# Optimization experiments

Measured on AMD Instinct MI355X. Metric: run time of the kernel, lower is better.

## Reference

```python
import jax, jax.numpy as jnp
import numpy as np

H = 16  # num_attention_heads
LN_EPS = 1e-12


def setup_inputs() -> dict:
    key = jax.random.key(0)
    ks = jax.random.split(key, 13)
    S, B, D = 2048, 2, 1024
    std = 0.02
    return {
        "query_tensor": jax.random.normal(ks[0], (S, B, D), jnp.float32),
        "key_tensor": jax.random.normal(ks[1], (S, B, D), jnp.float32),
        "value_tensor": jax.random.normal(ks[2], (S, B, D), jnp.float32),
        "Wq": jax.random.normal(ks[3], (D, D), jnp.float32) * std,
        "bq": jnp.zeros((D,), jnp.float32),
        "Wk": jax.random.normal(ks[4], (D, D), jnp.float32) * std,
        "bk": jnp.zeros((D,), jnp.float32),
        "Wv": jax.random.normal(ks[5], (D, D), jnp.float32) * std,
        "bv": jnp.zeros((D,), jnp.float32),
        "Wo": jax.random.normal(ks[6], (D, D), jnp.float32) * std,
        "bo": jnp.zeros((D,), jnp.float32),
        "ln_w": jnp.ones((D,), jnp.float32),
        "ln_b": jnp.zeros((D,), jnp.float32),
    }


def _layernorm(x, w, b):
    u = jnp.mean(x, axis=-1, keepdims=True)
    s = jnp.mean(jnp.square(x - u), axis=-1, keepdims=True)
    return w * ((x - u) / jnp.sqrt(s + LN_EPS)) + b


def reference(query_tensor, key_tensor, value_tensor, Wq, bq, Wk, bk, Wv, bv, Wo, bo, ln_w, ln_b):
    S, B, D = query_tensor.shape
    dh = D // H
    # QKV projections (nn.Linear: x @ W.T + b)
    q = query_tensor @ Wq.T + bq          # (S, B, D)
    k = key_tensor @ Wk.T + bk            # (Sk, B, D)
    v = value_tensor @ Wv.T + bv          # (Sk, B, D)
    # (S, B, D) -> (B*H, S, dh)
    q = q.reshape(S, B * H, dh).transpose(1, 0, 2)
    k = k.reshape(-1, B * H, dh).transpose(1, 0, 2)
    v = v.reshape(-1, B * H, dh).transpose(1, 0, 2)
    # NOTE: original code has NO 1/sqrt(dh) scaling
    scores = jnp.einsum('nqd,nkd->nqk', q, k)            # (B*H, S, Sk)
    probs = jax.nn.softmax(scores, axis=-1)
    # dropout is identity in eval mode
    ctx = jnp.einsum('nqk,nkd->nqd', probs, v)           # (B*H, S, dh)
    ctx = ctx.transpose(1, 0, 2).reshape(S, B, D)
    # BertSelfOutput: dense + residual + LayerNorm (dropout identity)
    out = ctx @ Wo.T + bo
    return _layernorm(out + query_tensor, ln_w, ln_b)
```

## Files before the change

### kernel.cpp

```cpp
#include <hip/hip_runtime.h>

#define SEQ    2048
#define BATCH  2
#define DMODEL 1024
#define NHEAD  16
#define DH     64
#define MROWS  (SEQ*BATCH)
#define RS     (BATCH*DMODEL)
#define LN_EPS 1e-12f
#define LOG2E  1.4426950408889634f

typedef __attribute__((ext_vector_type(8))) short short8;
typedef __attribute__((ext_vector_type(4))) float floatx4;

#define AS_GLOBAL __attribute__((address_space(1)))
#define AS_LDS    __attribute__((address_space(3)))

__device__ __forceinline__ float bf2f(unsigned short s) {
    union { unsigned u; float f; } a; a.u = ((unsigned)s) << 16; return a.f;
}
__device__ __forceinline__ unsigned short f2bf(float x) {
    union { float f; unsigned u; } a; a.f = x;
    unsigned r = a.u + 0x7fffu + ((a.u >> 16) & 1u);
    return (unsigned short)(r >> 16);
}
__device__ __forceinline__ unsigned cvt_pk_bf16(float a, float b) {
    unsigned r;
    asm("v_cvt_pk_bf16_f32 %0, %1, %2" : "=v"(r) : "v"(a), "v"(b));
    return r;
}
__device__ __forceinline__ float max3f(float a, float b, float c) {
    float r;
    asm("v_max3_f32 %0, %1, %2, %3" : "=v"(r) : "v"(a), "v"(b), "v"(c));
    return r;
}
__device__ __forceinline__ float fast_exp2(float x) {
#if __has_builtin(__builtin_amdgcn_exp2f)
    return __builtin_amdgcn_exp2f(x);
#else
    return exp2f(x);
#endif
}
__device__ __forceinline__ uint4 cvt8(const float* __restrict__ p) {
    float4 x0 = *(const float4*)(p);
    float4 x1 = *(const float4*)(p + 4);
    union { uint4 u; unsigned short s[8]; } r;
    r.s[0] = f2bf(x0.x); r.s[1] = f2bf(x0.y);
    r.s[2] = f2bf(x0.z); r.s[3] = f2bf(x0.w);
    r.s[4] = f2bf(x1.x); r.s[5] = f2bf(x1.y);
    r.s[6] = f2bf(x1.z); r.s[7] = f2bf(x1.w);
    return r.u;
}
__device__ __forceinline__ uint4 cvt8s(const float* __restrict__ p, float sc) {
    float4 x0 = *(const float4*)(p);
    float4 x1 = *(const float4*)(p + 4);
    union { uint4 u; unsigned short s[8]; } r;
    r.s[0] = f2bf(x0.x*sc); r.s[1] = f2bf(x0.y*sc);
    r.s[2] = f2bf(x0.z*sc); r.s[3] = f2bf(x0.w*sc);
    r.s[4] = f2bf(x1.x*sc); r.s[5] = f2bf(x1.y*sc);
    r.s[6] = f2bf(x1.z*sc); r.s[7] = f2bf(x1.w*sc);
    return r.u;
}

__global__ void beacon_kernel(float* out, float val) {
    if (threadIdx.x == 0) out[0] = val;
}

__global__ __launch_bounds__(256)
void cvt_kernel(const float* __restrict__ s0, const float* __restrict__ s1,
                const float* __restrict__ s2, const float* __restrict__ s3,
                const float* __restrict__ s4, const float* __restrict__ s5,
                const float* __restrict__ s6,
                unsigned short* __restrict__ d0, unsigned short* __restrict__ d1,
                unsigned short* __restrict__ d2, unsigned short* __restrict__ d3,
                unsigned short* __restrict__ d4, unsigned short* __restrict__ d5,
                unsigned short* __restrict__ d6)
{
    const float* srcs[7] = {s0, s1, s2, s3, s4, s5, s6};
    unsigned short* dsts[7] = {d0, d1, d2, d3, d4, d5, d6};
    const int cnts[7] = {4194304, 4194304, 4194304, 1048576, 1048576, 1048576, 1048576};
    const float scl[7] = {1.f, 1.f, 1.f, LOG2E, 1.f, 1.f, 1.f};
    const int z = blockIdx.z;
    const float* src = srcs[z];
    unsigned short* dst = dsts[z];
    const int count = cnts[z];
    const float sc = scl[z];
    const int stride = gridDim.x * 256 * 8;
    for (int i = (blockIdx.x * 256 + threadIdx.x) * 8; i < count; i += stride)
        *(uint4*)&dst[i] = cvt8s(&src[i], sc);
}

__global__ __launch_bounds__(256)
void vt_kernel(const unsigned short* __restrict__ Vb,
               unsigned short* __restrict__ VT)
{
    __shared__ __align__(16) short T[64*72];
    const int tid = threadIdx.x;
    const int s0 = blockIdx.x * 64;
    const int bh = blockIdx.y;
    const int b = bh >> 4, h = bh & 15;

    #pragma unroll
    for (int rep = 0; rep < 2; ++rep) {
        int c = tid + rep * 256;
        int s = c >> 3, cc = c & 7;
        *(uint4*)&T[s*72 + cc*8] =
            *(const uint4*)&Vb[((s0 + s) * BATCH + b) * DMODEL + h*64 + cc*8];
    }
    __syncthreads();
    #pragma unroll
    for (int rep = 0; rep < 2; ++rep) {
        int o = tid + rep * 256;
        int d = o >> 3, sc = o & 7;
        union { uint4 u; unsigned short e[8]; } pk;
        #pragma unroll
        for (int j = 0; j < 8; ++j)
            pk.e[j] = (unsigned short)T[(sc*8 + j)*72 + d];
        *(uint4*)&VT[bh*(DH*SEQ) + d*SEQ + s0 + sc*8] = pk.u;
    }
}

template<int OUTF32>
__device__ __forceinline__ void gemm_bf16_body(
    const unsigned short* __restrict__ A,
    const unsigned short* __restrict__ W,
    const float* __restrict__ bias, float bscale,
    void* __restrict__ Cout, int m0, int n0)
{
    __shared__ __align__(16) short Alds[2][128*32];
    __shared__ __align__(16) short Blds[2][128*32];

    const int tid  = threadIdx.x;
    const int lane = tid & 63;
    const int wave = tid >> 6;
    const int lrow = lane & 15;
    const int lq   = lane >> 4;
    const int mw = (wave >> 1) * 64;
    const int nw = (wave & 1) * 64;
    const int K  = DMODEL;

    const int chunk0 = tid;
    const int chunk1 = tid + 256;
    const int row0 = chunk0 >> 2, col0 = (chunk0 & 3) << 3;
    const int row1 = chunk1 >> 2, col1 = (chunk1 & 3) << 3;
    const unsigned short* gA0 = &A[(m0 + row0) * K + col0];
    const unsigned short* gA1 = &A[(m0 + row1) * K + col1];
    const unsigned short* gB0 = &W[(n0 + row0) * K + col0];
    const unsigned short* gB1 = &W[(n0 + row1) * K + col1];

    auto stage = [&](int k0, int b) {
        __builtin_amdgcn_global_load_lds((const AS_GLOBAL unsigned int*)(gA0 + k0),
            (AS_LDS unsigned int*)&Alds[b][(wave*64)*8], 16, 0, 0);
        __builtin_amdgcn_global_load_lds((const AS_GLOBAL unsigned int*)(gA1 + k0),
            (AS_LDS unsigned int*)&Alds[b][(256 + wave*64)*8], 16, 0, 0);
        __builtin_amdgcn_global_load_lds((const AS_GLOBAL unsigned int*)(gB0 + k0),
            (AS_LDS unsigned int*)&Blds[b][(wave*64)*8], 16, 0, 0);
        __builtin_amdgcn_global_load_lds((const AS_GLOBAL unsigned int*)(gB1 + k0),
            (AS_LDS unsigned int*)&Blds[b][(256 + wave*64)*8], 16, 0, 0);
    };

    floatx4 zero = {0.f, 0.f, 0.f, 0.f};
    floatx4 acc[4][4];
    #pragma unroll
    for (int i = 0; i < 4; ++i)
        #pragma unroll
        for (int j = 0; j < 4; ++j) acc[i][j] = zero;

    stage(0, 0);
    __syncthreads();

    for (int k0 = 0; k0 < K; k0 += 32) {
        const int cur = (k0 >> 5) & 1;
        if (k0 + 32 < K) stage(k0 + 32, cur ^ 1);
        short8 af[4], bfg[4];
        #pragma unroll
        for (int mi = 0; mi < 4; ++mi)
            af[mi] = *(const short8*)&Alds[cur][(mw + mi*16 + lrow)*32 + lq*8];
        #pragma unroll
        for (int ni = 0; ni < 4; ++ni)
            bfg[ni] = *(const short8*)&Blds[cur][(nw + ni*16 + lrow)*32 + lq*8];
        #pragma unroll
        for (int mi = 0; mi < 4; ++mi)
            #pragma unroll
            for (int ni = 0; ni < 4; ++ni)
                acc[mi][ni] = __builtin_amdgcn_mfma_f32_16x16x32_bf16(af[mi], bfg[ni], acc[mi][ni], 0, 0, 0);
        __syncthreads();
    }

    #pragma unroll
    for (int mi = 0; mi < 4; ++mi) {
        #pragma unroll
        for (int ni = 0; ni < 4; ++ni) {
            int n = n0 + nw + ni*16 + lrow;
            float bv_ = bias[n] * bscale;
            #pragma unroll
            for (int r = 0; r < 4; ++r) {
                int m = m0 + mw + mi*16 + lq*4 + r;
                float v = acc[mi][ni][r] + bv_;
                if (OUTF32) ((float*)Cout)[m * DMODEL + n] = v;
                else ((unsigned short*)Cout)[m * DMODEL + n] = f2bf(v);
            }
        }
    }
}

__global__ __launch_bounds__(256)
void qkv_bf16(const unsigned short* __restrict__ qb, const unsigned short* __restrict__ kb,
              const unsigned short* __restrict__ vb,
              const unsigned short* __restrict__ Wqb, const float* __restrict__ bq,
              const unsigned short* __restrict__ Wkb, const float* __restrict__ bk,
              const unsigned short* __restrict__ Wvb, const float* __restrict__ bv,
              unsigned short* __restrict__ Qo, unsigned short* __restrict__ Ko,
              unsigned short* __restrict__ Vo)
{
    const int flat = blockIdx.x;
    const int ns = (flat & 7) * 96 + (flat >> 3);
    const int z  = ns >> 8;
    const int r  = ns & 255;
    const int n0 = (r & 7) * 128;
    const int m0 = (r >> 3) * 128;

    const unsigned short *A, *W; const float* B; unsigned short* C; float bs;
    if (z == 0)      { A = qb; W = Wqb; B = bq; C = Qo; bs = LOG2E; }
    else if (z == 1) { A = kb; W = Wkb; B = bk; C = Ko; bs = 1.f; }
    else             { A = vb; W = Wvb; B = bv; C = Vo; bs = 1.f; }
    gemm_bf16_body<0>(A, W, B, bs, C, m0, n0);
}

__global__ __launch_bounds__(256)
void oproj_bf16(const unsigned short* __restrict__ Cx,
                const unsigned short* __restrict__ Wob, const float* __restrict__ bo,
                float* __restrict__ O32)
{
    const int flat = blockIdx.x;
    const int ns = (flat & 7) * 32 + (flat >> 3);
    const int n0 = (ns & 7) * 128;
    const int m0 = (ns >> 3) * 128;
    gemm_bf16_body<1>(Cx, Wob, bo, 1.f, O32, m0, n0);
}

__global__ __launch_bounds__(256)
void qkv_mfma(const float* __restrict__ q_in, const float* __restrict__ k_in,
              const float* __restrict__ v_in,
              const float* __restrict__ Wq, const float* __restrict__ bq,
              const float* __restrict__ Wk, const float* __restrict__ bk,
              const float* __restrict__ Wv, const float* __restrict__ bv,
              unsigned short* __restrict__ Qo, unsigned short* __restrict__ Ko,
              unsigned short* __restrict__ Vo)
{
    const float *A, *W, *B; unsigned short* C;
    if (blockIdx.z == 0)      { A = q_in; W = Wq; B = bq; C = Qo; }
    else if (blockIdx.z == 1) { A = k_in; W = Wk; B = bk; C = Ko; }
    else                      { A = v_in; W = Wv; B = bv; C = Vo; }

    __shared__ __align__(16) short Alds[128*32];
    __shared__ __align__(16) short Blds[128*32];
    const int tid  = threadIdx.x;
    const int lane = tid & 63;
    const int wave = tid >> 6;
    const int lrow = lane & 15;
    const int lq   = lane >> 4;
    const int m0 = blockIdx.x * 128;
    const int n0 = blockIdx.y * 128;
    const int mw = (wave >> 1) * 64;
    const int nw = (wave & 1) * 64;
    const int K  = DMODEL;

    floatx4 zero = {0.f, 0.f, 0.f, 0.f};
    floatx4 acc[4][4];
    #pragma unroll
    for (int i = 0; i < 4; ++i)
        #pragma unroll
        for (int j = 0; j < 4; ++j) acc[i][j] = zero;

    for (int k0 = 0; k0 < K; k0 += 32) {
        #pragma unroll
        for (int rep = 0; rep < 2; ++rep) {
            int chunk = tid + rep * 256;
            int row = chunk >> 2;
            int col = (chunk & 3) << 3;
            *(uint4*)&Alds[row*32 + col] = cvt8(&A[(m0 + row) * K + k0 + col]);
            *(uint4*)&Blds[row*32 + col] = cvt8(&W[(n0 + row) * K + k0 + col]);
        }
        __syncthreads();
        short8 af[4], bfg[4];
        #pragma unroll
        for (int mi = 0; mi < 4; ++mi)
            af[mi] = *(const short8*)&Alds[(mw + mi*16 + lrow)*32 + lq*8];
        #pragma unroll
        for (int ni = 0; ni < 4; ++ni)
            bfg[ni] = *(const short8*)&Blds[(nw + ni*16 + lrow)*32 + lq*8];
        #pragma unroll
        for (int mi = 0; mi < 4; ++mi)
            #pragma unroll
            for (int ni = 0; ni < 4; ++ni)
                acc[mi][ni] = __builtin_amdgcn_mfma_f32_16x16x32_bf16(af[mi], bfg[ni], acc[mi][ni], 0, 0, 0);
        __syncthreads();
    }

    #pragma unroll
    for (int mi = 0; mi < 4; ++mi) {
        #pragma unroll
        for (int ni = 0; ni < 4; ++ni) {
            int n = n0 + nw + ni*16 + lrow;
            float bv_ = B[n];
            #pragma unroll
            for (int r = 0; r < 4; ++r) {
                int m = m0 + mw + mi*16 + lq*4 + r;
                C[m * DMODEL + n] = f2bf(acc[mi][ni][r] + bv_);
            }
        }
    }
}

__global__ __launch_bounds__(256)
void oproj_mfma(const unsigned short* __restrict__ Cx,
                const float* __restrict__ Wo, const float* __restrict__ bo,
                float* __restrict__ O32)
{
    __shared__ __align__(16) short Alds[128*32];
    __shared__ __align__(16) short Blds[128*32];
    const int tid  = threadIdx.x;
    const int lane = tid & 63;
    const int wave = tid >> 6;
    const int lrow = lane & 15;
    const int lq   = lane >> 4;
    const int m0 = blockIdx.x * 128;
    const int n0 = blockIdx.y * 128;
    const int mw = (wave >> 1) * 64;
    const int nw = (wave & 1) * 64;
    const int K  = DMODEL;

    floatx4 zero = {0.f, 0.f, 0.f, 0.f};
    floatx4 acc[4][4];
    #pragma unroll
    for (int i = 0; i < 4; ++i)
        #pragma unroll
        for (int j = 0; j < 4; ++j) acc[i][j] = zero;

    for (int k0 = 0; k0 < K; k0 += 32) {
        #pragma unroll
        for (int rep = 0; rep < 2; ++rep) {
            int chunk = tid + rep * 256;
            int row = chunk >> 2;
            int col = (chunk & 3) << 3;
            *(uint4*)&Alds[row*32 + col] = *(const uint4*)&Cx[(m0 + row) * K + k0 + col];
            *(uint4*)&Blds[row*32 + col] = cvt8(&Wo[(n0 + row) * K + k0 + col]);
        }
        __syncthreads();
        short8 af[4], bfg[4];
        #pragma unroll
        for (int mi = 0; mi < 4; ++mi)
            af[mi] = *(const short8*)&Alds[(mw + mi*16 + lrow)*32 + lq*8];
        #pragma unroll
        for (int ni = 0; ni < 4; ++ni)
            bfg[ni] = *(const short8*)&Blds[(nw + ni*16 + lrow)*32 + lq*8];
        #pragma unroll
        for (int mi = 0; mi < 4; ++mi)
            #pragma unroll
            for (int ni = 0; ni < 4; ++ni)
                acc[mi][ni] = __builtin_amdgcn_mfma_f32_16x16x32_bf16(af[mi], bfg[ni], acc[mi][ni], 0, 0, 0);
        __syncthreads();
    }

    #pragma unroll
    for (int mi = 0; mi < 4; ++mi) {
        #pragma unroll
        for (int ni = 0; ni < 4; ++ni) {
            int n = n0 + nw + ni*16 + lrow;
            float bv_ = bo[n];
            #pragma unroll
            for (int r = 0; r < 4; ++r) {
                int m = m0 + mw + mi*16 + lq*4 + r;
                O32[m * DMODEL + n] = acc[mi][ni][r] + bv_;
            }
        }
    }
}

__global__ __launch_bounds__(256)
void attn_mfma6(const unsigned short* __restrict__ Q,
                const unsigned short* __restrict__ Kg,
                const unsigned short* __restrict__ VT,
                unsigned short* __restrict__ Ctx)
{
    __shared__ __align__(16) short SMEM[20480];

    const int tid  = threadIdx.x;
    const int lane = tid & 63;
    const int wave = tid >> 6;
    const int lrow = lane & 15;
    const int lq   = lane >> 4;

    const int flat = blockIdx.x + (blockIdx.y << 5);
    const int ns   = (flat & 7) * 128 + (flat >> 3);
    const int q0 = (ns & 31) * 64;
    const int bh = ns >> 5;

    const int off = (bh >> 4) * DMODEL + (bh & 15) * DH;
    const unsigned short* VTb = VT + bh * (DH * SEQ);
    short* const psw = &SMEM[16384 + wave * 1024];

    auto stageKV = [&](int kt, int b) {
        const int kbase = kt * 64;
        short* ksb = &SMEM[b * 8192];
        short* vtb = &SMEM[b * 8192 + 4096];
        #pragma unroll
        for (int rep = 0; rep < 2; ++rep) {
            int c = rep*256 + tid;
            int r = c >> 3, cc = c & 7;
            int sw = ((cc ^ (r & 7)) << 3);
            __builtin_amdgcn_global_load_lds(
                (const AS_GLOBAL unsigned int*)&Kg[(kbase + r) * RS + off + sw],
                (AS_LDS unsigned int*)&ksb[(rep*256 + wave*64) * 8], 16, 0, 0);
            __builtin_amdgcn_global_load_lds(
                (const AS_GLOBAL unsigned int*)&VTb[r * SEQ + kbase + sw],
                (AS_LDS unsigned int*)&vtb[(rep*256 + wave*64) * 8], 16, 0, 0);
        }
    };

    stageKV(0, 0);

    const int qrow = q0 + wave*16 + lrow;
    short8 qf[2];
    qf[0] = *(const short8*)&Q[qrow * RS + off + lq*8];
    qf[1] = *(const short8*)&Q[qrow * RS + off + 32 + lq*8];

    floatx4 zero = {0.f, 0.f, 0.f, 0.f};
    float m_i = -1e30f, l_i = 0.f;
    floatx4 oacc[4];
    #pragma unroll
    for (int ni = 0; ni < 4; ++ni) oacc[ni] = zero;

    __syncthreads();

    for (int kt = 0; kt < SEQ/64; ++kt) {
        const int cur = kt & 1;
        if (kt + 1 < SEQ/64) stageKV(kt + 1, cur ^ 1);
        const short* ksb = &SMEM[cur * 8192];
        const short* vtb = &SMEM[cur * 8192 + 4096];

        floatx4 sacc[4];
        #pragma unroll
        for (int ni = 0; ni < 4; ++ni) sacc[ni] = zero;
        __builtin_amdgcn_s_setprio(1);
        #pragma unroll
        for (int ni = 0; ni < 4; ++ni) {
            #pragma unroll
            for (int kk = 0; kk < 2; ++kk) {
                int key = ni*16 + lrow;
                int cc  = kk*4 + lq;
                short8 kf = *(const short8*)&ksb[key*64 + ((cc ^ (key & 7)) << 3)];
                sacc[ni] = __builtin_amdgcn_mfma_f32_16x16x32_bf16(kf, qf[kk], sacc[ni], 0, 0, 0);
            }
        }
        __builtin_amdgcn_s_setprio(0);

        float a0 = max3f(sacc[0][0], sacc[0][1], sacc[0][2]);
        float a1 = max3f(sacc[0][3], sacc[1][0], sacc[1][1]);
        float a2 = max3f(sacc[1][2], sacc[1][3], sacc[2][0]);
        float a3 = max3f(sacc[2][1], sacc[2][2], sacc[2][3]);
        float a4 = max3f(sacc[3][0], sacc[3][1], sacc[3][2]);
        float b0 = max3f(a0, a1, a2);
        float b1 = max3f(a3, a4, sacc[3][3]);
        float mx = fmaxf(b0, b1);
        mx = fmaxf(mx, __shfl_xor(mx, 16));
        mx = fmaxf(mx, __shfl_xor(mx, 32));

        if (!__all(mx <= m_i + 8.f)) {
            float mnew = fmaxf(m_i, mx);
            float alpha = fast_exp2(m_i - mnew);
            l_i *= alpha;
            #pragma unroll
            for (int ni = 0; ni < 4; ++ni)
                #pragma unroll
                for (int r = 0; r < 4; ++r) oacc[ni][r] *= alpha;
            m_i = mnew;
        }
        float p[4][4];
        #pragma unroll
        for (int ni = 0; ni < 4; ++ni)
            #pragma unroll
            for (int r = 0; r < 4; ++r)
                p[ni][r] = fast_exp2(sacc[ni][r] - m_i);

        float s00 = (p[0][0] + p[0][1]) + (p[0][2] + p[0][3]);
        float s01 = (p[1][0] + p[1][1]) + (p[1][2] + p[1][3]);
        float s10 = (p[2][0] + p[2][1]) + (p[2][2] + p[2][3]);
        float s11 = (p[3][0] + p[3][1]) + (p[3][2] + p[3][3]);
        float psum = (s00 + s01) + (s10 + s11);
        psum += __shfl_xor(psum, 16);
        psum += __shfl_xor(psum, 32);
        l_i += psum;

        #pragma unroll
        for (int ni = 0; ni < 4; ++ni) {
            uint2 pk;
            pk.x = cvt_pk_bf16(p[ni][0], p[ni][1]);
            pk.y = cvt_pk_bf16(p[ni][2], p[ni][3]);
            int t  = ni*2 + (lq >> 1);
            int tp = t ^ (lrow & 7);
            *(uint2*)&psw[lrow*64 + tp*8 + (lq & 1)*4] = pk;
        }
        __builtin_amdgcn_wave_barrier();

        short8 pf[2];
        #pragma unroll
        for (int kk = 0; kk < 2; ++kk) {
            int t  = kk*4 + lq;
            int tp = t ^ (lrow & 7);
            pf[kk] = *(const short8*)&psw[lrow*64 + tp*8];
        }

        __builtin_amdgcn_s_setprio(1);
        #pragma unroll
        for (int ni = 0; ni < 4; ++ni) {
            #pragma unroll
            for (int kk = 0; kk < 2; ++kk) {
                int d  = ni*16 + lrow;
                int cc = kk*4 + lq;
                short8 vf = *(const short8*)&vtb[d*64 + ((cc ^ (d & 7)) << 3)];
                oacc[ni] = __builtin_amdgcn_mfma_f32_16x16x32_bf16(vf, pf[kk], oacc[ni], 0, 0, 0);
            }
        }
        __builtin_amdgcn_s_setprio(0);

        __syncthreads();
    }

    const float inv = 1.f / l_i;
    #pragma unroll
    for (int ni = 0; ni < 4; ++ni) {
        uint2 ok;
        ok.x = cvt_pk_bf16(oacc[ni][0] * inv, oacc[ni][1] * inv);
        ok.y = cvt_pk_bf16(oacc[ni][2] * inv, oacc[ni][3] * inv);
        *(uint2*)&Ctx[qrow * RS + off + ni*16 + lq*4] = ok;
    }
}

__global__ __launch_bounds__(256)
void attn_mfma2(const unsigned short* __restrict__ Q,
                const unsigned short* __restrict__ Kg,
                const unsigned short* __restrict__ V,
                unsigned short* __restrict__ Ctx)
{
    __shared__ __align__(16) short Qs[64*72];
    __shared__ __align__(16) short Ks[64*72];
    __shared__ __align__(16) short Vt[64*72];
    __shared__ __align__(16) short Ps[4][16*72];

    const int tid  = threadIdx.x;
    const int lane = tid & 63;
    const int wave = tid >> 6;
    const int lrow = lane & 15;
    const int lq   = lane >> 4;

    const int q0 = blockIdx.x * 64;
    const int bh = blockIdx.y;
    const int off = (bh >> 4) * DMODEL + (bh & 15) * DH;

    #pragma unroll
    for (int rep = 0; rep < 2; ++rep) {
        int chunk = tid + rep * 256;
        int r = chunk >> 3;
        int c = (chunk & 7) << 3;
        *(uint4*)&Qs[r*72 + c] = *(const uint4*)&Q[(q0 + r) * RS + off + c];
    }
    __syncthreads();

    short8 qf[2];
    #pragma unroll
    for (int ks = 0; ks < 2; ++ks)
        qf[ks] = *(const short8*)&Qs[(wave*16 + lrow)*72 + ks*32 + lq*8];

    floatx4 zero = {0.f, 0.f, 0.f, 0.f};
    float m_i = -1e30f, l_i = 0.f;
    floatx4 oacc[4];
    #pragma unroll
    for (int ni = 0; ni < 4; ++ni) oacc[ni] = zero;

    for (int kt = 0; kt < SEQ/64; ++kt) {
        __syncthreads();
        const int kbase = kt * 64;
        #pragma unroll
        for (int rep = 0; rep < 2; ++rep) {
            int chunk = tid + rep * 256;
            int r = chunk >> 3;
            int c = (chunk & 7) << 3;
            *(uint4*)&Ks[r*72 + c] = *(const uint4*)&Kg[(kbase + r) * RS + off + c];
            uint4 vv = *(const uint4*)&V[(kbase + r) * RS + off + c];
            union { uint4 u; short s[8]; } uv; uv.u = vv;
            int swz = (chunk & 7) << 3;
            #pragma unroll
            for (int j = 0; j < 8; ++j)
                Vt[(c + j)*72 + (r ^ swz)] = uv.s[j];
        }
        __syncthreads();

        floatx4 sacc[4];
        #pragma unroll
        for (int ni = 0; ni < 4; ++ni) sacc[ni] = zero;
        #pragma unroll
        for (int ni = 0; ni < 4; ++ni) {
            #pragma unroll
            for (int ks = 0; ks < 2; ++ks) {
                short8 kf = *(const short8*)&Ks[(ni*16 + lrow)*72 + ks*32 + lq*8];
                sacc[ni] = __builtin_amdgcn_mfma_f32_16x16x32_bf16(kf, qf[ks], sacc[ni], 0, 0, 0);
            }
        }

        float mx = sacc[0][0];
        #pragma unroll
        for (int ni = 0; ni < 4; ++ni)
            #pragma unroll
            for (int r = 0; r < 4; ++r) mx = fmaxf(mx, sacc[ni][r]);
        mx = fmaxf(mx, __shfl_xor(mx, 16));
        mx = fmaxf(mx, __shfl_xor(mx, 32));
        float mnew = fmaxf(m_i, mx);
        float alpha = __expf(m_i - mnew);
        float p[4][4];
        float psum = 0.f;
        #pragma unroll
        for (int ni = 0; ni < 4; ++ni)
            #pragma unroll
            for (int r = 0; r < 4; ++r) {
                p[ni][r] = __expf(sacc[ni][r] - mnew);
                psum += p[ni][r];
            }
        psum += __shfl_xor(psum, 16);
        psum += __shfl_xor(psum, 32);
        l_i = l_i * alpha + psum;
        m_i = mnew;
        #pragma unroll
        for (int ni = 0; ni < 4; ++ni)
            #pragma unroll
            for (int r = 0; r < 4; ++r) oacc[ni][r] *= alpha;

        #pragma unroll
        for (int ni = 0; ni < 4; ++ni) {
            uint2 pk;
            pk.x = (unsigned)f2bf(p[ni][0]) | ((unsigned)f2bf(p[ni][1]) << 16);
            pk.y = (unsigned)f2bf(p[ni][2]) | ((unsigned)f2bf(p[ni][3]) << 16);
            *(uint2*)&Ps[wave][lrow*72 + ni*16 + lq*4] = pk;
        }
        __builtin_amdgcn_wave_barrier();

        short8 pf[2];
        #pragma unroll
        for (int ks = 0; ks < 2; ++ks)
            pf[ks] = *(const short8*)&Ps[wave][lrow*72 + ks*32 + lq*8];
        #pragma unroll
        for (int ni = 0; ni < 4; ++ni) {
            #pragma unroll
            for (int ks = 0; ks < 2; ++ks) {
                int d  = ni*16 + lrow;
                int kk = ks*32 + lq*8;
                int swz = ((d >> 3) & 7) << 3;
                short8 vf = *(const short8*)&Vt[d*72 + (kk ^ swz)];
                oacc[ni] = __builtin_amdgcn_mfma_f32_16x16x32_bf16(vf, pf[ks], oacc[ni], 0, 0, 0);
            }
        }
    }

    const float inv = 1.f / l_i;
    const int q = q0 + wave*16 + lrow;
    #pragma unroll
    for (int ni = 0; ni < 4; ++ni) {
        uint2 ok;
        ok.x = (unsigned)f2bf(oacc[ni][0] * inv) | ((unsigned)f2bf(oacc[ni][1] * inv) << 16);
        ok.y = (unsigned)f2bf(oacc[ni][2] * inv) | ((unsigned)f2bf(oacc[ni][3] * inv) << 16);
        *(uint2*)&Ctx[q * RS + off + ni*16 + lq*4] = ok;
    }
}

__global__ __launch_bounds__(256)
void ln2_kernel(const float* __restrict__ O,
                const float* __restrict__ resid,
                const float* __restrict__ w,
                const float* __restrict__ bb,
                float* __restrict__ out)
{
    __shared__ float r1s[4];
    __shared__ float r2s[4];
    const int row = blockIdx.x;
    const int tid = threadIdx.x;
    const int c4 = tid * 4;

    float4 o4 = *(const float4*)&O[row * DMODEL + c4];
    float4 q4 = *(const float4*)&resid[row * DMODEL + c4];
    float x0 = o4.x + q4.x;
    float x1 = o4.y + q4.y;
    float x2 = o4.z + q4.z;
    float x3 = o4.w + q4.w;

    float s1 = x0 + x1 + x2 + x3;
    float s2 = x0*x0 + x1*x1 + x2*x2 + x3*x3;
    #pragma unroll
    for (int o = 32; o > 0; o >>= 1) {
        s1 += __shfl_xor(s1, o);
        s2 += __shfl_xor(s2, o);
    }
    if ((tid & 63) == 0) { r1s[tid >> 6] = s1; r2s[tid >> 6] = s2; }
    __syncthreads();
    float t1 = r1s[0] + r1s[1] + r1s[2] + r1s[3];
    float t2 = r2s[0] + r2s[1] + r2s[2] + r2s[3];

    const float mean = t1 * (1.f / DMODEL);
    float var = t2 * (1.f / DMODEL) - mean * mean;
    var = fmaxf(var, 0.f);
    const float rstd = rsqrtf(var + LN_EPS);

    float4 w4 = *(const float4*)&w[c4];
    float4 b4 = *(const float4*)&bb[c4];
    float4 y;
    y.x = w4.x * ((x0 - mean) * rstd) + b4.x;
    y.y = w4.y * ((x1 - mean) * rstd) + b4.y;
    y.z = w4.z * ((x2 - mean) * rstd) + b4.z;
    y.w = w4.w * ((x3 - mean) * rstd) + b4.w;
    *(float4*)&out[row * DMODEL + c4] = y;
}

extern "C" void kernel_launch(void* const* d_in, const int* in_sizes, int n_in,
                              void* d_out, int out_size, void* d_ws, size_t ws_size,
                              hipStream_t stream) {
    const float* q_in = (const float*)d_in[0];
    const float* k_in = (const float*)d_in[1];
    const float* v_in = (const float*)d_in[2];
    const float* Wq = (const float*)d_in[3];  const float* bq = (const float*)d_in[4];
    const float* Wk = (const float*)d_in[5];  const float* bk = (const float*)d_in[6];
    const float* Wv = (const float*)d_in[7];  const float* bv = (const float*)d_in[8];
    const float* Wo = (const float*)d_in[9];  const float* bo = (const float*)d_in[10];
    const float* lnw = (const float*)d_in[11]; const float* lnb = (const float*)d_in[12];

    char* wsb = (char*)d_ws;
    unsigned short* QCtx = (unsigned short*)d_out;
    float*          outF = (float*)d_out;
    dim3 blk(256);

    if (ws_size >= (48u << 20)) {
        unsigned short* qb  = (unsigned short*)(wsb);
        unsigned short* kb  = (unsigned short*)(wsb + (8u  << 20));
        unsigned short* vb  = (unsigned short*)(wsb + (16u << 20));
        unsigned short* Wqb = (unsigned short*)(wsb + (24u << 20));
        unsigned short* Wkb = (unsigned short*)(wsb + (26u << 20));
        unsigned short* Wvb = (unsigned short*)(wsb + (28u << 20));
        unsigned short* Wob = (unsigned short*)(wsb + (30u << 20));
        unsigned short* Kb  = (unsigned short*)(wsb + (32u << 20));
        unsigned short* Vb  = (unsigned short*)(wsb + (40u << 20));
        unsigned short* VT  = (unsigned short*)(wsb);
        float*          O32 = (float*)(wsb);

        cvt_kernel<<<dim3(512, 1, 7), blk, 0, stream>>>(
            q_in, k_in, v_in, Wq, Wk, Wv, Wo,
            qb, kb, vb, Wqb, Wkb, Wvb, Wob);
        qkv_bf16<<<dim3(768), blk, 0, stream>>>(
            qb, kb, vb, Wqb, bq, Wkb, bk, Wvb, bv, QCtx, Kb, Vb);
        vt_kernel<<<dim3(SEQ/64, BATCH*NHEAD), blk, 0, stream>>>(Vb, VT);
        attn_mfma6<<<dim3(SEQ/64, BATCH*NHEAD), blk, 0, stream>>>(QCtx, Kb, VT, QCtx);
        oproj_bf16<<<dim3(256), blk, 0, stream>>>(QCtx, Wob, bo, O32);
        ln2_kernel<<<dim3(MROWS), blk, 0, stream>>>(O32, q_in, lnw, lnb, outF);
    } else if (ws_size >= (16u << 20)) {
        unsigned short* Kb  = (unsigned short*)(wsb);
        unsigned short* Vb  = (unsigned short*)(wsb + (8u << 20));
        float*          O32 = (float*)(wsb);
        qkv_mfma<<<dim3(MROWS/128, DMODEL/128, 3), blk, 0, stream>>>(
            q_in, k_in, v_in, Wq, bq, Wk, bk, Wv, bv, QCtx, Kb, Vb);
        attn_mfma2<<<dim3(SEQ/64, BATCH*NHEAD), blk, 0, stream>>>(QCtx, Kb, Vb, QCtx);
        oproj_mfma<<<dim3(MROWS/128, DMODEL/128), blk, 0, stream>>>(QCtx, Wo, bo, O32);
        ln2_kernel<<<dim3(MROWS), blk, 0, stream>>>(O32, q_in, lnw, lnb, outF);
    } else {
        beacon_kernel<<<1, 64, 0, stream>>>((float*)d_out, 300.0f);
    }
}
```

Measured before the change: 250.2 us.

## Double attention query tile per block to reuse staged K/V tiles

```diff
diff --git a/kernel.cpp b/kernel.cpp
--- a/kernel.cpp
+++ b/kernel.cpp
@@ -379,12 +379,13 @@
 }
 
 __global__ __launch_bounds__(256)
-void attn_mfma6(const unsigned short* __restrict__ Q,
+void attn_mfma7(const unsigned short* __restrict__ Q,
                 const unsigned short* __restrict__ Kg,
                 const unsigned short* __restrict__ VT,
                 unsigned short* __restrict__ Ctx)
 {
-    __shared__ __align__(16) short SMEM[20480];
+    __shared__ __align__(16) short SMEM[16384];
+    __shared__ __align__(16) short PS[8192];
 
     const int tid  = threadIdx.x;
     const int lane = tid & 63;
@@ -392,14 +393,13 @@
     const int lrow = lane & 15;
     const int lq   = lane >> 4;
 
-    const int flat = blockIdx.x + (blockIdx.y << 5);
-    const int ns   = (flat & 7) * 128 + (flat >> 3);
-    const int q0 = (ns & 31) * 64;
-    const int bh = ns >> 5;
+    const int flat = blockIdx.x;
+    const int ns   = (flat & 7) * 64 + (flat >> 3);
+    const int q0 = (ns & 15) * 128;
+    const int bh = ns >> 4;
 
     const int off = (bh >> 4) * DMODEL + (bh & 15) * DH;
     const unsigned short* VTb = VT + bh * (DH * SEQ);
-    short* const psw = &SMEM[16384 + wave * 1024];
 
     auto stageKV = [&](int kt, int b) {
         const int kbase = kt * 64;
@@ -421,16 +421,24 @@
 
     stageKV(0, 0);
 
-    const int qrow = q0 + wave*16 + lrow;
-    short8 qf[2];
-    qf[0] = *(const short8*)&Q[qrow * RS + off + lq*8];
-    qf[1] = *(const short8*)&Q[qrow * RS + off + 32 + lq*8];
+    int qrow[2];
+    qrow[0] = q0 + wave*32 + lrow;
+    qrow[1] = qrow[0] + 16;
+    short8 qf[2][2];
+    #pragma unroll
+    for (int s = 0; s < 2; ++s) {
+        qf[s][0] = *(const short8*)&Q[qrow[s] * RS + off + lq*8];
+        qf[s][1] = *(const short8*)&Q[qrow[s] * RS + off + 32 + lq*8];
+    }
 
     floatx4 zero = {0.f, 0.f, 0.f, 0.f};
-    float m_i = -1e30f, l_i = 0.f;
-    floatx4 oacc[4];
-    #pragma unroll
-    for (int ni = 0; ni < 4; ++ni) oacc[ni] = zero;
+    float m_i[2] = {-1e30f, -1e30f};
+    float l_i[2] = {0.f, 0.f};
+    floatx4 oacc[2][4];
+    #pragma unroll
+    for (int s = 0; s < 2; ++s)
+        #pragma unroll
+        for (int ni = 0; ni < 4; ++ni) oacc[s][ni] = zero;
 
     __syncthreads();
 
@@ -440,9 +448,11 @@
         const short* ksb = &SMEM[cur * 8192];
         const short* vtb = &SMEM[cur * 8192 + 4096];
 
-        floatx4 sacc[4];
-        #pragma unroll
-        for (int ni = 0; ni < 4; ++ni) sacc[ni] = zero;
+        floatx4 sacc[2][4];
+        #pragma unroll
+        for (int s = 0; s < 2; ++s)
+            #pragma unroll
+            for (int ni = 0; ni < 4; ++ni) sacc[s][ni] = zero;
         __builtin_amdgcn_s_setprio(1);
         #pragma unroll
         for (int ni = 0; ni < 4; ++ni) {
@@ -451,65 +461,84 @@
                 int key = ni*16 + lrow;
                 int cc  = kk*4 + lq;
                 short8 kf = *(const short8*)&ksb[key*64 + ((cc ^ (key & 7)) << 3)];
-                sacc[ni] = __builtin_amdgcn_mfma_f32_16x16x32_bf16(kf, qf[kk], sacc[ni], 0, 0, 0);
+                sacc[0][ni] = __builtin_amdgcn_mfma_f32_16x16x32_bf16(kf, qf[0][kk], sacc[0][ni], 0, 0, 0);
+                sacc[1][ni] = __builtin_amdgcn_mfma_f32_16x16x32_bf16(kf, qf[1][kk], sacc[1][ni], 0, 0, 0);
             }
         }
         __builtin_amdgcn_s_setprio(0);
 
-        float a0 = max3f(sacc[0][0], sacc[0][1], sacc[0][2]);
-        float a1 = max3f(sacc[0][3], sacc[1][0], sacc[1][1]);
-        float a2 = max3f(sacc[1][2], sacc[1][3], sacc[2][0]);
-        float a3 = max3f(sacc[2][1], sacc[2][2], sacc[2][3]);
-        float a4 = max3f(sacc[3][0], sacc[3][1], sacc[3][2]);
-        float b0 = max3f(a0, a1, a2);
-        float b1 = max3f(a3, a4, sacc[3][3]);
-        float mx = fmaxf(b0, b1);
-        mx = fmaxf(mx, __shfl_xor(mx, 16));
-        mx = fmaxf(mx, __shfl_xor(mx, 32));
-
-        if (!__all(mx <= m_i + 8.f)) {
-            float mnew = fmaxf(m_i, mx);
-            float alpha = fast_exp2(m_i - mnew);
-            l_i *= alpha;
+        float mx[2];
+        #pragma unroll
+        for (int s = 0; s < 2; ++s) {
+            float a0 = max3f(sacc[s][0][0], sacc[s][0][1], sacc[s][0][2]);
+            float a1 = max3f(sacc[s][0][3], sacc[s][1][0], sacc[s][1][1]);
+            float a2 = max3f(sacc[s][1][2], sacc[s][1][3], sacc[s][2][0]);
+            float a3 = max3f(sacc[s][2][1], sacc[s][2][2], sacc[s][2][3]);
+            float a4 = max3f(sacc[s][3][0], sacc[s][3][1], sacc[s][3][2]);
+            float b0 = max3f(a0, a1, a2);
+            float b1 = max3f(a3, a4, sacc[s][3][3]);
+            float m  = fmaxf(b0, b1);
+            m = fmaxf(m, __shfl_xor(m, 16));
+            m = fmaxf(m, __shfl_xor(m, 32));
+            mx[s] = m;
+        }
+
+        bool ok = (mx[0] <= m_i[0] + 8.f) && (mx[1] <= m_i[1] + 8.f);
+        if (!__all(ok)) {
+            #pragma unroll
+            for (int s = 0; s < 2; ++s) {
+                float mnew = fmaxf(m_i[s], mx[s]);
+                float alpha = fast_exp2(m_i[s] - mnew);
+                l_i[s] *= alpha;
+                #pragma unroll
+                for (int ni = 0; ni < 4; ++ni)
+                    #pragma unroll
+                    for (int r = 0; r < 4; ++r) oacc[s][ni][r] *= alpha;
+                m_i[s] = mnew;
+            }
+        }
+
+        #pragma unroll
+        for (int s = 0; s < 2; ++s) {
+            short* const psw = &PS[(wave*2 + s) * 1024];
+            float p[4][4];
             #pragma unroll
             for (int ni = 0; ni < 4; ++ni)
                 #pragma unroll
-                for (int r = 0; r < 4; ++r) oacc[ni][r] *= alpha;
-            m_i = mnew;
-        }
-        float p[4][4];
-        #pragma unroll
-        for (int ni = 0; ni < 4; ++ni)
-            #pragma unroll
-            for (int r = 0; r < 4; ++r)
-                p[ni][r] = fast_exp2(sacc[ni][r] - m_i);
-
-        float s00 = (p[0][0] + p[0][1]) + (p[0][2] + p[0][3]);
-        float s01 = (p[1][0] + p[1][1]) + (p[1][2] + p[1][3]);
-        float s10 = (p[2][0] + p[2][1]) + (p[2][2] + p[2][3]);
-        float s11 = (p[3][0] + p[3][1]) + (p[3][2] + p[3][3]);
-        float psum = (s00 + s01) + (s10 + s11);
-        psum += __shfl_xor(psum, 16);
-        psum += __shfl_xor(psum, 32);
-        l_i += psum;
-
-        #pragma unroll
-        for (int ni = 0; ni < 4; ++ni) {
-            uint2 pk;
-            pk.x = cvt_pk_bf16(p[ni][0], p[ni][1]);
-            pk.y = cvt_pk_bf16(p[ni][2], p[ni][3]);
-            int t  = ni*2 + (lq >> 1);
-            int tp = t ^ (lrow & 7);
-            *(uint2*)&psw[lrow*64 + tp*8 + (lq & 1)*4] = pk;
+                for (int r = 0; r < 4; ++r)
+                    p[ni][r] = fast_exp2(sacc[s][ni][r] - m_i[s]);
+
+            float s00 = (p[0][0] + p[0][1]) + (p[0][2] + p[0][3]);
+            float s01 = (p[1][0] + p[1][1]) + (p[1][2] + p[1][3]);
+            float s10 = (p[2][0] + p[2][1]) + (p[2][2] + p[2][3]);
+            float s11 = (p[3][0] + p[3][1]) + (p[3][2] + p[3][3]);
+            float psum = (s00 + s01) + (s10 + s11);
+            psum += __shfl_xor(psum, 16);
+            psum += __shfl_xor(psum, 32);
+            l_i[s] += psum;
+
+            #pragma unroll
+            for (int ni = 0; ni < 4; ++ni) {
+                uint2 pk;
+                pk.x = cvt_pk_bf16(p[ni][0], p[ni][1]);
+                pk.y = cvt_pk_bf16(p[ni][2], p[ni][3]);
+                int t  = ni*2 + (lq >> 1);
+                int tp = t ^ (lrow & 7);
+                *(uint2*)&psw[lrow*64 + tp*8 + (lq & 1)*4] = pk;
+            }
         }
         __builtin_amdgcn_wave_barrier();
 
-        short8 pf[2];
-        #pragma unroll
-        for (int kk = 0; kk < 2; ++kk) {
-            int t  = kk*4 + lq;
-            int tp = t ^ (lrow & 7);
-            pf[kk] = *(const short8*)&psw[lrow*64 + tp*8];
+        short8 pf[2][2];
+        #pragma unroll
+        for (int s = 0; s < 2; ++s) {
+            const short* const psw = &PS[(wave*2 + s) * 1024];
+            #pragma unroll
+            for (int kk = 0; kk < 2; ++kk) {
+                int t  = kk*4 + lq;
+                int tp = t ^ (lrow & 7);
+                pf[s][kk] = *(const short8*)&psw[lrow*64 + tp*8];
+            }
         }
 
         __builtin_amdgcn_s_setprio(1);
@@ -520,7 +549,8 @@
                 int d  = ni*16 + lrow;
                 int cc = kk*4 + lq;
                 short8 vf = *(const short8*)&vtb[d*64 + ((cc ^ (d & 7)) << 3)];
-                oacc[ni] = __builtin_amdgcn_mfma_f32_16x16x32_bf16(vf, pf[kk], oacc[ni], 0, 0, 0);
+                oacc[0][ni] = __builtin_amdgcn_mfma_f32_16x16x32_bf16(vf, pf[0][kk], oacc[0][ni], 0, 0, 0);
+                oacc[1][ni] = __builtin_amdgcn_mfma_f32_16x16x32_bf16(vf, pf[1][kk], oacc[1][ni], 0, 0, 0);
             }
         }
         __builtin_amdgcn_s_setprio(0);
@@ -528,13 +558,16 @@
         __syncthreads();
     }
 
-    const float inv = 1.f / l_i;
-    #pragma unroll
-    for (int ni = 0; ni < 4; ++ni) {
-        uint2 ok;
-        ok.x = cvt_pk_bf16(oacc[ni][0] * inv, oacc[ni][1] * inv);
-        ok.y = cvt_pk_bf16(oacc[ni][2] * inv, oacc[ni][3] * inv);
-        *(uint2*)&Ctx[qrow * RS + off + ni*16 + lq*4] = ok;
+    #pragma unroll
+    for (int s = 0; s < 2; ++s) {
+        const float inv = 1.f / l_i[s];
+        #pragma unroll
+        for (int ni = 0; ni < 4; ++ni) {
+            uint2 ok2;
+            ok2.x = cvt_pk_bf16(oacc[s][ni][0] * inv, oacc[s][ni][1] * inv);
+            ok2.y = cvt_pk_bf16(oacc[s][ni][2] * inv, oacc[s][ni][3] * inv);
+            *(uint2*)&Ctx[qrow[s] * RS + off + ni*16 + lq*4] = ok2;
+        }
     }
 }
 
@@ -756,7 +789,7 @@
         qkv_bf16<<<dim3(768), blk, 0, stream>>>(
             qb, kb, vb, Wqb, bq, Wkb, bk, Wvb, bv, QCtx, Kb, Vb);
         vt_kernel<<<dim3(SEQ/64, BATCH*NHEAD), blk, 0, stream>>>(Vb, VT);
-        attn_mfma6<<<dim3(SEQ/64, BATCH*NHEAD), blk, 0, stream>>>(QCtx, Kb, VT, QCtx);
+        attn_mfma7<<<dim3(512), blk, 0, stream>>>(QCtx, Kb, VT, QCtx);
         oproj_bf16<<<dim3(256), blk, 0, stream>>>(QCtx, Wob, bo, O32);
         ln2_kernel<<<dim3(MROWS), blk, 0, stream>>>(O32, q_in, lnw, lnb, outF);
     } else if (ws_size >= (16u << 20)) {
```

Result: no change. 251.6 us (+0.6%).
